# Kernel optimization log

Hardware: AMD Instinct MI355X
Metric: run time of the kernel (lower is better)

## Reference

```python
import jax, jax.numpy as jnp
import numpy as np

B, VOCAB, WD, ID = 128, 30000, 300, 2048
DROP_P = 0.5


def setup_inputs() -> dict:
    key = jax.random.key(0)
    k_im, k_w, k_emb, k_aw, k_ab, k_mask = jax.random.split(key, 6)
    ims = jax.random.normal(k_im, (B, ID), dtype=jnp.float32)
    words = jax.random.randint(k_w, (B,), 0, VOCAB, dtype=jnp.int64)
    embed_w = jax.random.normal(k_emb, (VOCAB, WD), dtype=jnp.float32)
    align_w = jax.random.normal(k_aw, (2, WD * ID), dtype=jnp.float32) * 0.01
    align_b = jax.random.normal(k_ab, (2,), dtype=jnp.float32)
    # inverted dropout mask: bernoulli(keep) / keep, matching nn.Dropout(p=0.5)
    keep = 1.0 - DROP_P
    drop_mask = (jax.random.bernoulli(k_mask, keep, (B, WD * ID)).astype(jnp.float32) / keep)
    return {"ims": ims, "words": words, "embed_w": embed_w,
            "align_w": align_w, "align_b": align_b, "drop_mask": drop_mask}


def reference(ims, words, embed_w, align_w, align_b, drop_mask):
    wv = embed_w[words]                                   # [B, WD] embedding lookup
    # outer product per sample: [B, WD, 1] x [B, 1, ID] -> [B, WD*ID]
    feat = (wv[:, :, None] * ims[:, None, :]).reshape(wv.shape[0], -1)
    feat = feat * drop_mask                               # dropout
    return feat @ align_w.T + align_b                     # [B, 2]
```

## Files before the change

kernel.cpp:

```cpp
#include <hip/hip_runtime.h>

#define NB    128
#define WD    300
#define IDIM  2048
#define FEAT  (WD * IDIM)
#define CHUNKS 16
#define VECS_TOTAL   (FEAT / 4)
#define VECS_CHUNK   (VECS_TOTAL / CHUNKS)
#define THREADS 256

__global__ void init_out_kernel(const float* __restrict__ align_b,
                                float* __restrict__ out) {
    int t = threadIdx.x;
    out[t] = align_b[t & 1];
}

__global__ __launch_bounds__(THREADS)
void oan_reduce_kernel(const float* __restrict__ ims,
                       const int*   __restrict__ words,
                       const float* __restrict__ embed_w,
                       const float* __restrict__ align_w,
                       const float* __restrict__ drop,
                       float* __restrict__ out)
{
    __shared__ float s_ims[IDIM];
    __shared__ float s_wv[WD];
    __shared__ float s_red[8];

    const int b     = blockIdx.y;
    const int chunk = blockIdx.x;
    const int tid   = threadIdx.x;

    const float4* ims4   = (const float4*)(ims + (size_t)b * IDIM);
    float4*       s_ims4 = (float4*)s_ims;
    for (int v = tid; v < IDIM / 4; v += THREADS) s_ims4[v] = ims4[v];
    const float* wvp = embed_w + (size_t)words[b] * WD;
    for (int w = tid; w < WD; w += THREADS) s_wv[w] = wvp[w];
    __syncthreads();

    const float4* dm4 = (const float4*)(drop + (size_t)b * FEAT);
    const float4* aw0 = (const float4*)(align_w);
    const float4* aw1 = (const float4*)(align_w + FEAT);

    float acc0 = 0.f, acc1 = 0.f;
    const int v0 = chunk * VECS_CHUNK;
    for (int v = v0 + tid; v < v0 + VECS_CHUNK; v += THREADS) {
        const int k  = v << 2;
        const float wv = s_wv[k >> 11];
        const float4 im = s_ims4[(k & (IDIM - 1)) >> 2];
        const float4 d  = dm4[v];
        const float4 a0 = aw0[v];
        const float4 a1 = aw1[v];
        const float p0 = wv * im.x * d.x;
        const float p1 = wv * im.y * d.y;
        const float p2 = wv * im.z * d.z;
        const float p3 = wv * im.w * d.w;
        acc0 += p0 * a0.x + p1 * a0.y + p2 * a0.z + p3 * a0.w;
        acc1 += p0 * a1.x + p1 * a1.y + p2 * a1.z + p3 * a1.w;
    }

    #pragma unroll
    for (int off = 32; off > 0; off >>= 1) {
        acc0 += __shfl_down(acc0, off, 64);
        acc1 += __shfl_down(acc1, off, 64);
    }
    const int lane = tid & 63;
    const int wave = tid >> 6;
    if (lane == 0) { s_red[wave * 2] = acc0; s_red[wave * 2 + 1] = acc1; }
    __syncthreads();
    if (tid == 0) {
        const float t0 = s_red[0] + s_red[2] + s_red[4] + s_red[6];
        const float t1 = s_red[1] + s_red[3] + s_red[5] + s_red[7];
        atomicAdd(&out[b * 2 + 0], t0);
        atomicAdd(&out[b * 2 + 1], t1);
    }
}

extern "C" void kernel_launch(void* const* d_in, const int* in_sizes, int n_in,
                              void* d_out, int out_size, void* d_ws, size_t ws_size,
                              hipStream_t stream) {
    const float* ims     = (const float*)d_in[0];
    const int*   words   = (const int*)  d_in[1];
    const float* embed_w = (const float*)d_in[2];
    const float* align_w = (const float*)d_in[3];
    const float* align_b = (const float*)d_in[4];
    const float* drop    = (const float*)d_in[5];
    float* out = (float*)d_out;

    init_out_kernel<<<1, 256, 0, stream>>>(align_b, out);
    dim3 grid(CHUNKS, NB);
    oan_reduce_kernel<<<grid, THREADS, 0, stream>>>(ims, words, embed_w,
                                                    align_w, drop, out);
}
```

Before: 450.9 us.

## Process two batch rows per block, hoist image vectors to registers, unroll

Each block now handles two samples, so every align_w vector load serves both rows and halves weight traffic. Because the per-thread stride wraps the image dimension, the needed image vectors are loaded once into registers, which removes per-iteration shared-memory reads. The dropout mask is read with nontemporal loads and the loop is unrolled by two to keep more loads in flight. The chunk count doubles so the total block count stays the same, at the cost of more registers per thread.

```diff
diff --git a/kernel.cpp b/kernel.cpp
--- a/kernel.cpp
+++ b/kernel.cpp
@@ -4,10 +4,12 @@
 #define WD    300
 #define IDIM  2048
 #define FEAT  (WD * IDIM)
-#define CHUNKS 16
-#define VECS_TOTAL   (FEAT / 4)
-#define VECS_CHUNK   (VECS_TOTAL / CHUNKS)
+#define VECS  (FEAT / 4)
+#define CHUNKS 32
+#define VCH   (VECS / CHUNKS)
 #define THREADS 256
+
+typedef float f32x4 __attribute__((ext_vector_type(4)));
 
 __global__ void init_out_kernel(const float* __restrict__ align_b,
                                 float* __restrict__ out) {
@@ -16,63 +18,89 @@
 }
 
 __global__ __launch_bounds__(THREADS)
-void oan_reduce_kernel(const float* __restrict__ ims,
-                       const int*   __restrict__ words,
-                       const float* __restrict__ embed_w,
-                       const float* __restrict__ align_w,
-                       const float* __restrict__ drop,
-                       float* __restrict__ out)
+void oan_reduce2_kernel(const float* __restrict__ ims,
+                        const int*   __restrict__ words,
+                        const float* __restrict__ embed_w,
+                        const float* __restrict__ align_w,
+                        const float* __restrict__ drop,
+                        float* __restrict__ out)
 {
-    __shared__ float s_ims[IDIM];
-    __shared__ float s_wv[WD];
-    __shared__ float s_red[8];
+    __shared__ float s_wv[2][WD];
+    __shared__ float s_red[16];
 
-    const int b     = blockIdx.y;
     const int chunk = blockIdx.x;
+    const int b0    = blockIdx.y * 2;
+    const int b1    = b0 + 1;
     const int tid   = threadIdx.x;
 
-    const float4* ims4   = (const float4*)(ims + (size_t)b * IDIM);
-    float4*       s_ims4 = (float4*)s_ims;
-    for (int v = tid; v < IDIM / 4; v += THREADS) s_ims4[v] = ims4[v];
-    const float* wvp = embed_w + (size_t)words[b] * WD;
-    for (int w = tid; w < WD; w += THREADS) s_wv[w] = wvp[w];
+    const float* wv0p = embed_w + (size_t)words[b0] * WD;
+    const float* wv1p = embed_w + (size_t)words[b1] * WD;
+    for (int w = tid; w < WD; w += THREADS) {
+        s_wv[0][w] = wv0p[w];
+        s_wv[1][w] = wv1p[w];
+    }
+
+    const f32x4* imr0 = (const f32x4*)(ims + (size_t)b0 * IDIM);
+    const f32x4* imr1 = (const f32x4*)(ims + (size_t)b1 * IDIM);
+    const int v0   = chunk * VCH;
+    int       v    = v0 + tid;
+    const int vend = v0 + VCH;
+    const f32x4 imA0 = imr0[v & 511];
+    const f32x4 imA1 = imr1[v & 511];
+    const f32x4 imB0 = imr0[(v + 256) & 511];
+    const f32x4 imB1 = imr1[(v + 256) & 511];
     __syncthreads();
 
-    const float4* dm4 = (const float4*)(drop + (size_t)b * FEAT);
-    const float4* aw0 = (const float4*)(align_w);
-    const float4* aw1 = (const float4*)(align_w + FEAT);
+    const f32x4* dm0 = (const f32x4*)(drop + (size_t)b0 * FEAT);
+    const f32x4* dm1 = (const f32x4*)(drop + (size_t)b1 * FEAT);
+    const f32x4* aw0 = (const f32x4*)(align_w);
+    const f32x4* aw1 = (const f32x4*)(align_w + FEAT);
 
-    float acc0 = 0.f, acc1 = 0.f;
-    const int v0 = chunk * VECS_CHUNK;
-    for (int v = v0 + tid; v < v0 + VECS_CHUNK; v += THREADS) {
-        const int k  = v << 2;
-        const float wv = s_wv[k >> 11];
-        const float4 im = s_ims4[(k & (IDIM - 1)) >> 2];
-        const float4 d  = dm4[v];
-        const float4 a0 = aw0[v];
-        const float4 a1 = aw1[v];
-        const float p0 = wv * im.x * d.x;
-        const float p1 = wv * im.y * d.y;
-        const float p2 = wv * im.z * d.z;
-        const float p3 = wv * im.w * d.w;
-        acc0 += p0 * a0.x + p1 * a0.y + p2 * a0.z + p3 * a0.w;
-        acc1 += p0 * a1.x + p1 * a1.y + p2 * a1.z + p3 * a1.w;
+    float a00 = 0.f, a01 = 0.f, a10 = 0.f, a11 = 0.f;
+
+#define BODY(VV, IM0, IM1) {                                                  \
+        const float  w0 = s_wv[0][(VV) >> 9];                                 \
+        const float  w1 = s_wv[1][(VV) >> 9];                                 \
+        const f32x4 d0 = __builtin_nontemporal_load(&dm0[VV]);                \
+        const f32x4 d1 = __builtin_nontemporal_load(&dm1[VV]);                \
+        const f32x4 g0 = aw0[VV];                                             \
+        const f32x4 g1 = aw1[VV];                                             \
+        float p0 = w0 * (IM0).x * d0.x, p1 = w0 * (IM0).y * d0.y;             \
+        float p2 = w0 * (IM0).z * d0.z, p3 = w0 * (IM0).w * d0.w;             \
+        a00 += p0 * g0.x + p1 * g0.y + p2 * g0.z + p3 * g0.w;                 \
+        a01 += p0 * g1.x + p1 * g1.y + p2 * g1.z + p3 * g1.w;                 \
+        p0 = w1 * (IM1).x * d1.x; p1 = w1 * (IM1).y * d1.y;                   \
+        p2 = w1 * (IM1).z * d1.z; p3 = w1 * (IM1).w * d1.w;                   \
+        a10 += p0 * g0.x + p1 * g0.y + p2 * g0.z + p3 * g0.w;                 \
+        a11 += p0 * g1.x + p1 * g1.y + p2 * g1.z + p3 * g1.w;                 \
     }
+
+    for (; v + 256 < vend; v += 512) {
+        BODY(v,       imA0, imA1);
+        BODY(v + 256, imB0, imB1);
+    }
+    if (v < vend) BODY(v, imA0, imA1);
+#undef BODY
 
     #pragma unroll
     for (int off = 32; off > 0; off >>= 1) {
-        acc0 += __shfl_down(acc0, off, 64);
-        acc1 += __shfl_down(acc1, off, 64);
+        a00 += __shfl_down(a00, off, 64);
+        a01 += __shfl_down(a01, off, 64);
+        a10 += __shfl_down(a10, off, 64);
+        a11 += __shfl_down(a11, off, 64);
     }
     const int lane = tid & 63;
     const int wave = tid >> 6;
-    if (lane == 0) { s_red[wave * 2] = acc0; s_red[wave * 2 + 1] = acc1; }
+    if (lane == 0) {
+        s_red[wave * 4 + 0] = a00;
+        s_red[wave * 4 + 1] = a01;
+        s_red[wave * 4 + 2] = a10;
+        s_red[wave * 4 + 3] = a11;
+    }
     __syncthreads();
-    if (tid == 0) {
-        const float t0 = s_red[0] + s_red[2] + s_red[4] + s_red[6];
-        const float t1 = s_red[1] + s_red[3] + s_red[5] + s_red[7];
-        atomicAdd(&out[b * 2 + 0], t0);
-        atomicAdd(&out[b * 2 + 1], t1);
+    if (tid < 4) {
+        const float t = s_red[tid] + s_red[4 + tid] + s_red[8 + tid] + s_red[12 + tid];
+        atomicAdd(&out[b0 * 2 + tid], t);
     }
 }
 
@@ -88,7 +116,7 @@
     float* out = (float*)d_out;
 
     init_out_kernel<<<1, 256, 0, stream>>>(align_b, out);
-    dim3 grid(CHUNKS, NB);
-    oan_reduce_kernel<<<grid, THREADS, 0, stream>>>(ims, words, embed_w,
-                                                    align_w, drop, out);
+    dim3 grid(CHUNKS, NB / 2);
+    oan_reduce2_kernel<<<grid, THREADS, 0, stream>>>(ims, words, embed_w,
+                                                     align_w, drop, out);
 }
```

Result: faster. 424.1 us (-5.9%).
